# Optimization experiments

Hardware: AMD Instinct MI355X
Metric: run time of the kernel (lower is better)

Reference implementation:

```python
import jax, jax.numpy as jnp
import numpy as np
from jax import lax

T, D, H = 8192, 1024, 1024
FORGET_BIAS = 1.0  # BasicLSTMCell default


def setup_inputs() -> dict:
    key = jax.random.key(0)
    ks = jax.random.split(key, 5)
    x = jax.random.normal(ks[0], (T, D), dtype=jnp.float32)
    c_in = jax.random.normal(ks[1], (1, H), dtype=jnp.float32)
    h_in = jax.random.normal(ks[2], (1, H), dtype=jnp.float32)
    # BasicLSTMCell kernel [D+H, 4H], gates ordered (i, j, f, o); glorot-ish scale
    W_lstm = jax.random.normal(ks[3], (D + H, 4 * H), dtype=jnp.float32) * (1.0 / np.sqrt(D + H))
    b_lstm = jnp.zeros((4 * H,), dtype=jnp.float32)
    # normc_initializer(1.0): columns normalized to unit norm
    W_out = jax.random.normal(ks[4], (H, H), dtype=jnp.float32)
    W_out = W_out / jnp.linalg.norm(W_out, axis=0, keepdims=True)
    b_out = jnp.zeros((H,), dtype=jnp.float32)
    return {"x": x, "c_in": c_in, "h_in": h_in, "W_lstm": W_lstm,
            "b_lstm": b_lstm, "W_out": W_out, "b_out": b_out}


def reference(x, c_in, h_in, W_lstm, b_lstm, W_out, b_out):
    # Precompute the input contribution for all timesteps in one big GEMM;
    # the recurrence only needs the h @ W_h part per step.
    Wx, Wh = W_lstm[:D], W_lstm[D:]          # [D,4H], [H,4H]
    xz = x @ Wx + b_lstm                      # [T, 4H]

    def step(carry, xz_t):
        c, h = carry                          # [H], [H]
        z = xz_t + h @ Wh                     # [4H]
        i, j, f, o = jnp.split(z, 4)
        new_c = c * jax.nn.sigmoid(f + FORGET_BIAS) + jax.nn.sigmoid(i) * jnp.tanh(j)
        new_h = jnp.tanh(new_c) * jax.nn.sigmoid(o)
        return (new_c, new_h), new_h

    (c_last, h_last), hs = lax.scan(step, (c_in[0], h_in[0]), xz)  # hs: [T, H]
    output = hs @ W_out + b_out               # final_layer (no activation)
    return output, c_last[None, :], h_last[None, :]
```

## Files before the change

### kernel.cpp

```cpp
#include <hip/hip_runtime.h>

#define T_STEPS 8192
#define DD 1024
#define HH 1024
#define NWG 256
#define NTHR 512
#define SCOPE_AGENT __HIP_MEMORY_SCOPE_AGENT
typedef unsigned long long u64;

__device__ __forceinline__ int swz(int k) { return k ^ ((((k) >> 6) & 3) << 2); }

__device__ __forceinline__ float fsig(float v) {
  return 1.f / (1.f + __expf(-v));
}
__device__ __forceinline__ float ftanh(float v) {
  return 2.f / (1.f + __expf(-2.f * v)) - 1.f;
}

__global__ __launch_bounds__(NTHR, 1) void lstm_scan(
    const float* __restrict__ x, const float* __restrict__ c_in,
    const float* __restrict__ h_in, const float* __restrict__ W,
    const float* __restrict__ b, float* __restrict__ Hs,
    u64* __restrict__ hbuf,
    float* __restrict__ out_tail)
{
  const int g = blockIdx.x, tid = threadIdx.x;
  const int lane = tid & 63, wave = tid >> 6;
  const int col = tid & 15, seg = tid >> 4;
  const int gate = col >> 2, hi = col & 3;
  const int cg = gate * HH + g * 4 + hi;

  __shared__ float Wl[32768];
  __shared__ float xb[DD];
  __shared__ float hb[HH];
  __shared__ float partial[8][16];

  float c_reg = 0.f, hlast = 0.f;

  if (tid < 4) {
    const float h0 = h_in[g * 4 + tid];
    c_reg = c_in[g * 4 + tid];
    const u64 pv = ((u64)1u << 32) | (u64)__float_as_uint(h0);
    __hip_atomic_store(&hbuf[g * 4 + tid], pv, __ATOMIC_RELAXED, SCOPE_AGENT);
  }

  #pragma unroll
  for (int j = 0; j < 16; ++j) {
    float4 v;
    v.x = W[(size_t)(seg * 64 + j * 4 + 0) * (4 * HH) + cg];
    v.y = W[(size_t)(seg * 64 + j * 4 + 1) * (4 * HH) + cg];
    v.z = W[(size_t)(seg * 64 + j * 4 + 2) * (4 * HH) + cg];
    v.w = W[(size_t)(seg * 64 + j * 4 + 3) * (4 * HH) + cg];
    *(float4*)&Wl[(wave * 16 + j) * 256 + lane * 4] = v;
  }

  const float bias_reg = b[((lane & 15) >> 2) * HH + g * 4 + (lane & 3)];

  float xv0 = x[tid], xv1 = x[tid + 512];

  __syncthreads();

  const bool is_x = (seg < 16);
  const int s2 = seg - 16;

  for (int t = 1; t <= T_STEPS; ++t) {
    xb[swz(tid)]       = xv0;
    xb[swz(tid + 512)] = xv1;
    __syncthreads();

    if (t < T_STEPS) {
      const float* xn = x + (size_t)t * DD;
      xv0 = xn[tid];
      xv1 = xn[tid + 512];
    }
    if (is_x) {
      float p = 0.f;
      #pragma unroll
      for (int j = 0; j < 16; ++j) {
        const float4 wv = *(const float4*)&Wl[(wave * 16 + j) * 256 + lane * 4];
        const float4 xv = *(const float4*)&xb[(seg * 64 + j * 4) ^ ((seg & 3) << 2)];
        p = fmaf(xv.x, wv.x, p); p = fmaf(xv.y, wv.y, p);
        p = fmaf(xv.z, wv.z, p); p = fmaf(xv.w, wv.w, p);
      }
      p += __shfl_xor(p, 16);
      p += __shfl_xor(p, 32);
      if (lane < 16) partial[wave][lane] = p;
    }

    {
      const u64* hp = hbuf + ((t - 1) & 1) * HH;
      u64 v0 = __hip_atomic_load(&hp[tid],       __ATOMIC_RELAXED, SCOPE_AGENT);
      u64 v1 = __hip_atomic_load(&hp[tid + 512], __ATOMIC_RELAXED, SCOPE_AGENT);
      bool r0 = (unsigned)(v0 >> 32) >= (unsigned)t;
      bool r1 = (unsigned)(v1 >> 32) >= (unsigned)t;
      while (!(r0 && r1)) {
        __builtin_amdgcn_s_sleep(1);
        if (!r0) {
          v0 = __hip_atomic_load(&hp[tid], __ATOMIC_RELAXED, SCOPE_AGENT);
          r0 = (unsigned)(v0 >> 32) >= (unsigned)t;
        }
        if (!r1) {
          v1 = __hip_atomic_load(&hp[tid + 512], __ATOMIC_RELAXED, SCOPE_AGENT);
          r1 = (unsigned)(v1 >> 32) >= (unsigned)t;
        }
      }
      hb[swz(tid)]       = __uint_as_float((unsigned)v0);
      hb[swz(tid + 512)] = __uint_as_float((unsigned)v1);
    }
    __syncthreads();

    if (!is_x) {
      float q = 0.f;
      #pragma unroll
      for (int j = 0; j < 16; ++j) {
        const float4 wv = *(const float4*)&Wl[(wave * 16 + j) * 256 + lane * 4];
        const float4 hv = *(const float4*)&hb[(s2 * 64 + j * 4) ^ ((s2 & 3) << 2)];
        q = fmaf(hv.x, wv.x, q); q = fmaf(hv.y, wv.y, q);
        q = fmaf(hv.z, wv.z, q); q = fmaf(hv.w, wv.w, q);
      }
      q += __shfl_xor(q, 16);
      q += __shfl_xor(q, 32);
      if (lane < 16) partial[wave][lane] = q;
    }
    __syncthreads();

    if (wave == 0) {
      float zsum = bias_reg;
      #pragma unroll
      for (int wv = 0; wv < 8; ++wv) zsum += partial[wv][lane & 15];
      const float zi = __shfl(zsum, tid);
      const float zj = __shfl(zsum, tid + 4);
      const float zf = __shfl(zsum, tid + 8);
      const float zo = __shfl(zsum, tid + 12);
      if (tid < 4) {
        const float fg = fsig(zf + 1.0f);
        const float nc = c_reg * fg + fsig(zi) * ftanh(zj);
        const float nh = ftanh(nc) * fsig(zo);
        c_reg = nc; hlast = nh;
        const u64 pv = ((u64)(unsigned)(t + 1) << 32) | (u64)__float_as_uint(nh);
        __hip_atomic_store(&hbuf[(t & 1) * HH + g * 4 + tid], pv,
                           __ATOMIC_RELAXED, SCOPE_AGENT);
        Hs[(size_t)(t - 1) * HH + g * 4 + tid] = nh;
      }
    }
  }

  if (tid < 4) {
    out_tail[g * 4 + tid]      = c_reg;
    out_tail[HH + g * 4 + tid] = hlast;
  }
}

#define BM 64
#define BN 64
#define BK 16
__global__ __launch_bounds__(256, 2) void out_gemm(
    const float* __restrict__ A,
    const float* __restrict__ Bw,
    const float* __restrict__ bias,
    float* __restrict__ C)
{
  __shared__ float As[BM][BK];
  __shared__ float Bs[BK][BN];
  const int tid = threadIdx.x;
  const int row0 = blockIdx.y * BM, col0 = blockIdx.x * BN;
  const int tx = tid & 15, ty = tid >> 4;

  float acc[4][4];
  #pragma unroll
  for (int j = 0; j < 4; ++j) {
    const float bv = bias[col0 + tx * 4 + j];
    #pragma unroll
    for (int i = 0; i < 4; ++i) acc[i][j] = bv;
  }

  for (int k0 = 0; k0 < HH; k0 += BK) {
    {
      const int r = tid >> 2, c = (tid & 3) * 4;
      const float4 va = *(const float4*)&A[(size_t)(row0 + r) * HH + k0 + c];
      As[r][c] = va.x; As[r][c + 1] = va.y; As[r][c + 2] = va.z; As[r][c + 3] = va.w;
      const int rb = tid >> 4, cb = (tid & 15) * 4;
      *(float4*)&Bs[rb][cb] = *(const float4*)&Bw[(size_t)(k0 + rb) * HH + col0 + cb];
    }
    __syncthreads();
    #pragma unroll
    for (int kk = 0; kk < BK; ++kk) {
      float a[4], bv[4];
      #pragma unroll
      for (int i = 0; i < 4; ++i) a[i] = As[ty * 4 + i][kk];
      #pragma unroll
      for (int j = 0; j < 4; ++j) bv[j] = Bs[kk][tx * 4 + j];
      #pragma unroll
      for (int i = 0; i < 4; ++i)
        #pragma unroll
        for (int j = 0; j < 4; ++j)
          acc[i][j] = fmaf(a[i], bv[j], acc[i][j]);
    }
    __syncthreads();
  }

  #pragma unroll
  for (int i = 0; i < 4; ++i) {
    float4 v = make_float4(acc[i][0], acc[i][1], acc[i][2], acc[i][3]);
    *(float4*)&C[(size_t)(row0 + ty * 4 + i) * HH + col0 + tx * 4] = v;
  }
}

extern "C" void kernel_launch(void* const* d_in, const int* in_sizes, int n_in,
                              void* d_out, int out_size, void* d_ws, size_t ws_size,
                              hipStream_t stream) {
  const float* x    = (const float*)d_in[0];
  const float* c_in = (const float*)d_in[1];
  const float* h_in = (const float*)d_in[2];
  const float* W    = (const float*)d_in[3];
  const float* b    = (const float*)d_in[4];
  const float* Wout = (const float*)d_in[5];
  const float* bout = (const float*)d_in[6];
  float* out = (float*)d_out;

  u64* hbuf = (u64*)d_ws;
  float* Hs = (float*)(hbuf + 2 * HH);
  float* out_tail = out + (size_t)T_STEPS * HH;

  hipMemsetAsync(hbuf, 0, 2 * HH * sizeof(u64), stream);

  void* args[] = {(void*)&x, (void*)&c_in, (void*)&h_in, (void*)&W, (void*)&b,
                  (void*)&Hs, (void*)&hbuf, (void*)&out_tail};
  hipLaunchCooperativeKernel((void*)lstm_scan, dim3(NWG), dim3(NTHR),
                             args, 0, stream);

  out_gemm<<<dim3(HH / BN, T_STEPS / BM), 256, 0, stream>>>(Hs, Wout, bout, out);
}
```

Baseline: 16.14 ms.

## Split x and h work across waves and drop a barrier in the LSTM step

The x-projection waves (0-3) and h-projection waves (4-7) now run in separate branches. Each h wave polls only the 256 hidden entries it consumes and writes them to LDS itself, followed by an explicit LDS waitcnt, which removes one block-wide __syncthreads per timestep. The poll loop no longer sleeps. The gate activations are computed in parallel across 16 lanes with a single exp each, using tanh(x) = 2*sigmoid(2x) - 1, instead of serially in 4 lanes. The risk is hotter spinning on the flags and reliance on wave-local LDS visibility, which holds only because each h wave reads back exactly the hb entries it wrote.

```diff
diff --git a/kernel.cpp b/kernel.cpp
--- a/kernel.cpp
+++ b/kernel.cpp
@@ -60,8 +60,7 @@
 
   __syncthreads();
 
-  const bool is_x = (seg < 16);
-  const int s2 = seg - 16;
+  const bool is_x = (wave < 4);
 
   for (int t = 1; t <= T_STEPS; ++t) {
     xb[swz(tid)]       = xv0;
@@ -73,6 +72,7 @@
       xv0 = xn[tid];
       xv1 = xn[tid + 512];
     }
+
     if (is_x) {
       float p = 0.f;
       #pragma unroll
@@ -85,31 +85,30 @@
       p += __shfl_xor(p, 16);
       p += __shfl_xor(p, 32);
       if (lane < 16) partial[wave][lane] = p;
-    }
-
-    {
+    } else {
       const u64* hp = hbuf + ((t - 1) & 1) * HH;
-      u64 v0 = __hip_atomic_load(&hp[tid],       __ATOMIC_RELAXED, SCOPE_AGENT);
-      u64 v1 = __hip_atomic_load(&hp[tid + 512], __ATOMIC_RELAXED, SCOPE_AGENT);
-      bool r0 = (unsigned)(v0 >> 32) >= (unsigned)t;
-      bool r1 = (unsigned)(v1 >> 32) >= (unsigned)t;
-      while (!(r0 && r1)) {
-        __builtin_amdgcn_s_sleep(1);
-        if (!r0) {
-          v0 = __hip_atomic_load(&hp[tid], __ATOMIC_RELAXED, SCOPE_AGENT);
-          r0 = (unsigned)(v0 >> 32) >= (unsigned)t;
-        }
-        if (!r1) {
-          v1 = __hip_atomic_load(&hp[tid + 512], __ATOMIC_RELAXED, SCOPE_AGENT);
-          r1 = (unsigned)(v1 >> 32) >= (unsigned)t;
-        }
-      }
-      hb[swz(tid)]       = __uint_as_float((unsigned)v0);
-      hb[swz(tid + 512)] = __uint_as_float((unsigned)v1);
-    }
-    __syncthreads();
-
-    if (!is_x) {
+      const int cb = (wave - 4) * 256;
+      const unsigned tg = (unsigned)t;
+      u64 a0 = __hip_atomic_load(&hp[cb + lane],       __ATOMIC_RELAXED, SCOPE_AGENT);
+      u64 a1 = __hip_atomic_load(&hp[cb + 64 + lane],  __ATOMIC_RELAXED, SCOPE_AGENT);
+      u64 a2 = __hip_atomic_load(&hp[cb + 128 + lane], __ATOMIC_RELAXED, SCOPE_AGENT);
+      u64 a3 = __hip_atomic_load(&hp[cb + 192 + lane], __ATOMIC_RELAXED, SCOPE_AGENT);
+      bool r0 = (unsigned)(a0 >> 32) >= tg;
+      bool r1 = (unsigned)(a1 >> 32) >= tg;
+      bool r2 = (unsigned)(a2 >> 32) >= tg;
+      bool r3 = (unsigned)(a3 >> 32) >= tg;
+      while (!(r0 & r1 & r2 & r3)) {
+        if (!r0) { a0 = __hip_atomic_load(&hp[cb + lane],       __ATOMIC_RELAXED, SCOPE_AGENT); r0 = (unsigned)(a0 >> 32) >= tg; }
+        if (!r1) { a1 = __hip_atomic_load(&hp[cb + 64 + lane],  __ATOMIC_RELAXED, SCOPE_AGENT); r1 = (unsigned)(a1 >> 32) >= tg; }
+        if (!r2) { a2 = __hip_atomic_load(&hp[cb + 128 + lane], __ATOMIC_RELAXED, SCOPE_AGENT); r2 = (unsigned)(a2 >> 32) >= tg; }
+        if (!r3) { a3 = __hip_atomic_load(&hp[cb + 192 + lane], __ATOMIC_RELAXED, SCOPE_AGENT); r3 = (unsigned)(a3 >> 32) >= tg; }
+      }
+      hb[swz(cb + lane)]       = __uint_as_float((unsigned)a0);
+      hb[swz(cb + 64 + lane)]  = __uint_as_float((unsigned)a1);
+      hb[swz(cb + 128 + lane)] = __uint_as_float((unsigned)a2);
+      hb[swz(cb + 192 + lane)] = __uint_as_float((unsigned)a3);
+      asm volatile("s_waitcnt lgkmcnt(0)" ::: "memory");
+      const int s2 = seg - 16;
       float q = 0.f;
       #pragma unroll
       for (int j = 0; j < 16; ++j) {
@@ -128,14 +127,17 @@
       float zsum = bias_reg;
       #pragma unroll
       for (int wv = 0; wv < 8; ++wv) zsum += partial[wv][lane & 15];
-      const float zi = __shfl(zsum, tid);
-      const float zj = __shfl(zsum, tid + 4);
-      const float zf = __shfl(zsum, tid + 8);
-      const float zo = __shfl(zsum, tid + 12);
+      const int gt = (lane & 15) >> 2;
+      const float zin = (gt == 1) ? (2.f * zsum) : (gt == 2 ? zsum + 1.f : zsum);
+      const float s = 1.f / (1.f + __expf(-zin));
+      const float act = (gt == 1) ? (2.f * s - 1.f) : s;
+      const float ig = __shfl(act, tid);
+      const float tj = __shfl(act, tid + 4);
+      const float fg = __shfl(act, tid + 8);
+      const float og = __shfl(act, tid + 12);
       if (tid < 4) {
-        const float fg = fsig(zf + 1.0f);
-        const float nc = c_reg * fg + fsig(zi) * ftanh(zj);
-        const float nh = ftanh(nc) * fsig(zo);
+        const float nc = c_reg * fg + ig * tj;
+        const float nh = ftanh(nc) * og;
         c_reg = nc; hlast = nh;
         const u64 pv = ((u64)(unsigned)(t + 1) << 32) | (u64)__float_as_uint(nh);
         __hip_atomic_store(&hbuf[(t & 1) * HH + g * 4 + tid], pv,
```

After: 12.97 ms. -19.6%, faster.
